# Optimization experiments

Measured on AMD Instinct MI355X. Metric: run time of the kernel, lower is better.

## Reference

```python
import jax, jax.numpy as jnp
import numpy as np

MARGIN = 0.075
CONF_THRESHOLD = 0.2


def setup_inputs() -> dict:
    key = jax.random.key(0)
    k1, k2, k3 = jax.random.split(key, 3)
    N, D = 32768, 256
    embeddings = jax.random.normal(k1, (N, D), dtype=jnp.float32)
    tags = jax.random.randint(k2, (N,), 0, 500, dtype=jnp.int64)
    confidences = jax.random.uniform(k3, (N,), dtype=jnp.float32)
    return {"embeddings": embeddings, "tags": tags, "confidences": confidences}


def _safe_sqrt(sq):
    # gradient-safe sqrt: zero at sq<=0 (matches d(0)=0, avoids NaN in vjp)
    pos = sq > 0
    return jnp.where(pos, jnp.sqrt(jnp.where(pos, sq, 1.0)), 0.0)


def _triplet_hard_mining(emb, labels):
    n = emb.shape[0]
    # pairwise euclidean distances (cdist p=2)
    sq_norm = jnp.sum(emb * emb, axis=1)  # [n]
    sq = sq_norm[:, None] + sq_norm[None, :] - 2.0 * (emb @ emb.T)
    dist = _safe_sqrt(jnp.maximum(sq, 0.0))  # [n, n]

    same = labels[:, None] == labels[None, :]
    eye = jnp.eye(n, dtype=bool)
    pos_mask = same & ~eye
    neg_mask = ~same

    inf = jnp.float32(jnp.inf)
    hard_pos = jnp.max(jnp.where(pos_mask, dist, -inf), axis=1)  # [n]
    neg_min = jnp.min(jnp.where(neg_mask, dist, inf), axis=1)    # [n]
    # semi-hard negatives: neg dists strictly greater than hardest positive
    shn_mask = neg_mask & (dist > hard_pos[:, None])
    shn_min = jnp.min(jnp.where(shn_mask, dist, inf), axis=1)
    hard_neg = jnp.where(jnp.isfinite(shn_min), shn_min, neg_min)

    valid = jnp.any(pos_mask, axis=1) & jnp.any(neg_mask, axis=1)
    per_anchor = jax.nn.relu(hard_pos - hard_neg + MARGIN)
    per_anchor = jnp.where(valid, per_anchor, 0.0)
    cnt = jnp.sum(valid.astype(jnp.float32))
    # if no valid anchors (also covers <2 unique labels), loss is 0
    return jnp.where(cnt > 0, jnp.sum(per_anchor) / jnp.maximum(cnt, 1.0), 0.0)


def reference(embeddings, tags, confidences):
    n = embeddings.shape[0]
    top_k = int(CONF_THRESHOLD * n)
    _, idx = jax.lax.top_k(confidences, top_k)
    emb = embeddings[idx]
    labels = tags[idx]
    return _triplet_hard_mining(emb, labels)
```

## Files before the change

### kernel.cpp

```cpp
#include <hip/hip_runtime.h>
#include <math.h>

#define D 256
#define MARGIN 0.075f
#define MAXM 96

typedef __bf16 bf8_t __attribute__((ext_vector_type(8)));
typedef float f4_t __attribute__((ext_vector_type(4)));
typedef int i4_t __attribute__((ext_vector_type(4)));
typedef unsigned long long ull;

#define AS1 __attribute__((address_space(1)))
#define AS3 __attribute__((address_space(3)))
static __device__ __forceinline__ void gload_lds16(const void* g, void* s) {
    __builtin_amdgcn_global_load_lds((const AS1 unsigned int*)g, (AS3 unsigned int*)s, 16, 0, 0);
}

static __device__ __forceinline__ unsigned short f2bf(float x) {
    unsigned u = __float_as_uint(x);
    unsigned r = (u + 0x7fffu + ((u >> 16) & 1u)) >> 16;
    return (unsigned short)r;
}

static __device__ __forceinline__ float dec_min(unsigned cm) {
    return (cm == 0u) ? __builtin_inff() : __uint_as_float(~cm);
}

static __device__ __forceinline__ float rmin16(float v) {
    int s;
    s = __builtin_amdgcn_update_dpp(__float_as_int(v), __float_as_int(v), 0x101, 0xF, 0xF, false);
    v = fminf(v, __int_as_float(s));
    s = __builtin_amdgcn_update_dpp(__float_as_int(v), __float_as_int(v), 0x102, 0xF, 0xF, false);
    v = fminf(v, __int_as_float(s));
    s = __builtin_amdgcn_update_dpp(__float_as_int(v), __float_as_int(v), 0x104, 0xF, 0xF, false);
    v = fminf(v, __int_as_float(s));
    s = __builtin_amdgcn_update_dpp(__float_as_int(v), __float_as_int(v), 0x108, 0xF, 0xF, false);
    v = fminf(v, __int_as_float(s));
    return v;
}

__global__ __launch_bounds__(256) void k_histscan(const float* __restrict__ conf,
                                                  int n, int ksel,
                                                  unsigned* __restrict__ h1,
                                                  unsigned* __restrict__ ctrl) {
    int t = threadIdx.x;
    int i = blockIdx.x * 256 + t;
    if (i < n) atomicAdd(&h1[__float_as_uint(conf[i]) >> 16], 1u);
    __threadfence();
    __syncthreads();
    __shared__ unsigned sdone;
    if (t == 0) sdone = atomicAdd(&ctrl[8], 1u);
    __syncthreads();
    if (sdone != gridDim.x - 1) return;
    __threadfence();
    __shared__ unsigned part[256], sfx[256];
    __shared__ int schunk;
    unsigned k = (unsigned)ksel;
    unsigned s = 0;
    const uint4* h4 = (const uint4*)(h1 + t * 256);
    #pragma unroll
    for (int b = 0; b < 64; b++) { uint4 v = h4[b]; s += v.x + v.y + v.z + v.w; }
    part[t] = s;
    __syncthreads();
    for (int off = 1; off < 256; off <<= 1) {
        unsigned v = (t + off < 256) ? part[t + off] : 0u;
        __syncthreads();
        part[t] += v;
        __syncthreads();
    }
    if (part[t] >= k && (t == 255 || part[t + 1] < k)) schunk = t;
    __syncthreads();
    int c = schunk;
    unsigned above = (c == 255) ? 0u : part[c + 1];
    sfx[t] = h1[c * 256 + t];
    __syncthreads();
    for (int off = 1; off < 256; off <<= 1) {
        unsigned v = (t + off < 256) ? sfx[t + off] : 0u;
        __syncthreads();
        sfx[t] += v;
        __syncthreads();
    }
    if (above + sfx[t] >= k && (t == 255 || above + sfx[t + 1] < k)) {
        unsigned gt = above + ((t == 255) ? 0u : sfx[t + 1]);
        ctrl[3] = (unsigned)(c * 256 + t);
        ctrl[1] = gt;
        ctrl[2] = k - gt;
    }
}

__global__ __launch_bounds__(256) void k_selrank(const float* __restrict__ conf, int n,
                                                 unsigned* __restrict__ ctrl,
                                                 int* __restrict__ idx_sel,
                                                 ull* __restrict__ cand) {
    int t = threadIdx.x;
    int i = blockIdx.x * 256 + t;
    unsigned b16 = ctrl[3];
    if (i < n) {
        unsigned u = __float_as_uint(conf[i]);
        unsigned t16 = u >> 16;
        if (t16 > b16) {
            unsigned pos = atomicAdd(&ctrl[5], 1u);
            idx_sel[pos] = i;
        } else if (t16 == b16) {
            unsigned pos = atomicAdd(&ctrl[6], 1u);
            __hip_atomic_store(&cand[pos], ((ull)u << 32) | (unsigned)i,
                               __ATOMIC_RELAXED, __HIP_MEMORY_SCOPE_AGENT);
        }
    }
    __threadfence();
    __syncthreads();
    __shared__ unsigned sdone;
    if (t == 0) sdone = atomicAdd(&ctrl[9], 1u);
    __syncthreads();
    if (sdone != gridDim.x - 1) return;
    __threadfence();

    __shared__ ull scand[1024];
    int M = (int)__hip_atomic_load(&ctrl[6], __ATOMIC_RELAXED, __HIP_MEMORY_SCOPE_AGENT);
    unsigned need = ctrl[2], cgt = ctrl[1];
    bool useLds = (M <= 1024);
    if (useLds) {
        for (int m = t; m < M; m += 256)
            scand[m] = __hip_atomic_load(&cand[m], __ATOMIC_RELAXED, __HIP_MEMORY_SCOPE_AGENT);
        __syncthreads();
    }
    for (int j = t; j < M; j += 256) {
        ull cj = useLds ? scand[j]
                        : __hip_atomic_load(&cand[j], __ATOMIC_RELAXED, __HIP_MEMORY_SCOPE_AGENT);
        unsigned uj = (unsigned)(cj >> 32);
        unsigned rank = 0;
        for (int m = 0; m < M; m++) {
            ull cm = useLds ? scand[m]
                            : __hip_atomic_load(&cand[m], __ATOMIC_RELAXED, __HIP_MEMORY_SCOPE_AGENT);
            unsigned um = (unsigned)(cm >> 32);
            if (um > uj || (um == uj && cm < cj)) rank++;
        }
        if (rank < need) idx_sel[cgt + rank] = (int)(unsigned)(cj & 0xFFFFFFFFu);
    }
}

__global__ void k_gather(const float* __restrict__ emb, const int* __restrict__ tags,
                         const int* __restrict__ idx_sel, int ksel, int np,
                         unsigned short* __restrict__ ebf, float* __restrict__ sqn,
                         int* __restrict__ lsel, unsigned* __restrict__ labhist,
                         int* __restrict__ members) {
    int j = blockIdx.x;
    int t = threadIdx.x;
    if (j < ksel) {
        int src = idx_sel[j];
        float4 v = *(const float4*)&emb[(size_t)src * D + t * 4];
        ushort4 o;
        o.x = f2bf(v.x); o.y = f2bf(v.y); o.z = f2bf(v.z); o.w = f2bf(v.w);
        *(ushort4*)&ebf[(size_t)j * D + t * 4] = o;
        float s = v.x * v.x + v.y * v.y + v.z * v.z + v.w * v.w;
        for (int off = 32; off > 0; off >>= 1) s += __shfl_down(s, off);
        if (t == 0) {
            int lab = tags[src];
            sqn[j] = s; lsel[j] = lab;
            unsigned slot = atomicAdd(&labhist[lab], 1u);
            if (slot < MAXM) members[lab * MAXM + slot] = j;
        }
    } else {
        ushort4 z = {0, 0, 0, 0};
        *(ushort4*)&ebf[(size_t)j * D + t * 4] = z;
        if (t == 0) { sqn[j] = __builtin_inff(); lsel[j] = -1; }
    }
}

__global__ __launch_bounds__(256) void k_hardpos(const unsigned short* __restrict__ ebf,
                                                 const float* __restrict__ sqn,
                                                 const int* __restrict__ members,
                                                 const unsigned* __restrict__ labhist,
                                                 unsigned* __restrict__ hp_g) {
    int L = blockIdx.x;
    int t = threadIdx.x;
    int m = (int)labhist[L];
    if (m > MAXM) m = MAXM;
    if (m < 2) return;

    __shared__ unsigned short rows[MAXM * 256];
    __shared__ float lsqn[MAXM];
    __shared__ unsigned hpl[MAXM];
    __shared__ int ridx[MAXM];

    for (int a = t; a < m; a += 256) {
        int r = members[L * MAXM + a];
        ridx[a] = r; lsqn[a] = sqn[r]; hpl[a] = 0u;
    }
    __syncthreads();
    for (int e = t * 8; e < m * 256; e += 256 * 8) {
        int a = e >> 8, c = e & 255;
        *(uint4*)&rows[a * 256 + c] = *(const uint4*)&ebf[(size_t)ridx[a] * D + c];
    }
    __syncthreads();

    int npair = m * (m - 1) / 2;
    for (int pidx = t; pidx < npair; pidx += 256) {
        int a = 0, rem = pidx;
        while (rem >= m - 1 - a) { rem -= m - 1 - a; a++; }
        int b = a + 1 + rem;
        const unsigned* ra = (const unsigned*)&rows[a * 256];
        const unsigned* rb = (const unsigned*)&rows[b * 256];
        float dot = 0.f;
        #pragma unroll 8
        for (int c = 0; c < 128; c++) {
            unsigned ua = ra[c], ub = rb[c];
            float a0 = __uint_as_float(ua << 16);
            float a1 = __uint_as_float(ua & 0xFFFF0000u);
            float b0 = __uint_as_float(ub << 16);
            float b1 = __uint_as_float(ub & 0xFFFF0000u);
            dot = fmaf(a0, b0, dot);
            dot = fmaf(a1, b1, dot);
        }
        float dsq = fmaxf(lsqn[a] + lsqn[b] - 2.f * dot, 0.f);
        unsigned bits = __float_as_uint(dsq);
        atomicMax(&hpl[a], bits);
        atomicMax(&hpl[b], bits);
    }
    __syncthreads();
    for (int a = t; a < m; a += 256) hp_g[ridx[a]] = hpl[a];
}

__global__ __launch_bounds__(256, 3) void k_fused(const unsigned short* __restrict__ Ebf,
                                                  const float* __restrict__ sqn,
                                                  const int* __restrict__ lsel,
                                                  const unsigned* __restrict__ hp_g,
                                                  unsigned* __restrict__ nm_g,
                                                  unsigned* __restrict__ shn_g,
                                                  int np, int nb, int ksel) {
    int rem = blockIdx.x, bi = 0;
    while (rem >= nb - bi) { rem -= nb - bi; bi++; }
    int bj = bi + rem;
    int i0 = bi * 128, j0 = bj * 128;
    bool diag = (bi == bj);

    __shared__ __align__(16) char smem[32768];
    char* ldsA = smem;
    char* ldsB = smem + 16384;

    int t = threadIdx.x;
    int w = t >> 6, l = t & 63;
    int wm = w & 1, wn = w >> 1;
    int lr = l & 15, lq = l >> 4;
    int r7 = lr & 7, rh = lr >> 3;

    int dr = l >> 3;
    int sg = (l & 7) ^ dr;
    const unsigned short* gA = Ebf + (size_t)(i0 + dr) * D + sg * 8;
    const unsigned short* gB = Ebf + (size_t)(j0 + dr) * D + sg * 8;

    f4_t zero = {0.f, 0.f, 0.f, 0.f};
    f4_t acc[4][4];
    #pragma unroll
    for (int p = 0; p < 4; p++)
        #pragma unroll
        for (int q = 0; q < 4; q++) acc[p][q] = zero;

    for (int k0 = 0; k0 < D; k0 += 64) {
        #pragma unroll
        for (int c = 0; c < 4; c++) {
            int R0 = w * 32 + c * 8;
            gload_lds16(gA + (size_t)R0 * D + k0, ldsA + R0 * 128);
            gload_lds16(gB + (size_t)R0 * D + k0, ldsB + R0 * 128);
        }
        __syncthreads();
        #pragma unroll
        for (int ks8 = 0; ks8 < 8; ks8 += 4) {
            bf8_t a[4], b[4];
            #pragma unroll
            for (int p = 0; p < 4; p++) {
                int off = ((wm * 8 + p * 2 + rh) << 10) + ((r7 * 8 + ((ks8 + lq) ^ r7)) << 4);
                a[p] = *(const bf8_t*)(ldsA + off);
            }
            #pragma unroll
            for (int q = 0; q < 4; q++) {
                int off = ((wn * 8 + q * 2 + rh) << 10) + ((r7 * 8 + ((ks8 + lq) ^ r7)) << 4);
                b[q] = *(const bf8_t*)(ldsB + off);
            }
            #pragma unroll
            for (int p = 0; p < 4; p++)
                #pragma unroll
                for (int q = 0; q < 4; q++)
                    acc[p][q] = __builtin_amdgcn_mfma_f32_16x16x32_bf16(a[p], b[q], acc[p][q], 0, 0, 0);
        }
        __syncthreads();
    }

    float* sqnA = (float*)smem;
    float* sqnB = sqnA + 128;
    int* labA = (int*)(sqnB + 128);
    int* labB = labA + 128;
    float* thrA = (float*)(labB + 128);
    float* thrB = thrA + 128;
    if (t < 128) {
        float s = sqn[i0 + t];
        sqnA[t] = s; labA[t] = lsel[i0 + t];
        thrA[t] = __uint_as_float(hp_g[i0 + t]) - s;
    } else {
        int u = t - 128;
        float s = sqn[j0 + u];
        sqnB[u] = s; labB[u] = lsel[j0 + u];
        thrB[u] = __uint_as_float(hp_g[j0 + u]) - s;
    }
    __syncthreads();

    const float INF = __builtin_inff();
    int colL[4], ljv[4];
    float sBq[4], thrBq[4];
    #pragma unroll
    for (int q = 0; q < 4; q++) {
        colL[q] = wn * 64 + q * 16 + lr;
        ljv[q] = labB[colL[q]];
        sBq[q] = sqnB[colL[q]];
        thrBq[q] = thrB[colL[q]];
    }
    f4_t sqA4[4], thrA4[4];
    i4_t labA4[4];
    #pragma unroll
    for (int p = 0; p < 4; p++) {
        int rb = wm * 64 + p * 16 + lq * 4;
        sqA4[p] = *(const f4_t*)&sqnA[rb];
        thrA4[p] = *(const f4_t*)&thrA[rb];
        labA4[p] = *(const i4_t*)&labA[rb];
    }

    #pragma unroll
    for (int p = 0; p < 4; p++) {
        #pragma unroll
        for (int r = 0; r < 4; r++) {
            int li = labA4[p][r];
            float thr = thrA4[p][r];
            float nmv = INF, smv = INF;
            #pragma unroll
            for (int q = 0; q < 4; q++) {
                float v = fmaf(-2.f, acc[p][q][r], sBq[q]);
                v = (ljv[q] == li) ? INF : v;
                nmv = fminf(nmv, v);
                smv = fminf(smv, (v > thr) ? v : INF);
            }
            nmv = rmin16(nmv);
            smv = rmin16(smv);
            if (lr == 0) {
                int gm = i0 + wm * 64 + p * 16 + lq * 4 + r;
                float sqi = sqA4[p][r];
                if (nmv < INF)
                    atomicMax(&nm_g[gm], ~__float_as_uint(fmaxf(sqi + nmv, 0.f)));
                if (smv < INF)
                    atomicMax(&shn_g[gm], ~__float_as_uint(fmaxf(sqi + smv, 0.f)));
            }
        }
    }

    if (!diag) {
        #pragma unroll
        for (int q = 0; q < 4; q++) {
            int lj = ljv[q];
            float thrc = thrBq[q];
            float nmv = INF, smv = INF;
            #pragma unroll
            for (int p = 0; p < 4; p++)
                #pragma unroll
                for (int r = 0; r < 4; r++) {
                    float w2 = fmaf(-2.f, acc[p][q][r], sqA4[p][r]);
                    w2 = (labA4[p][r] == lj) ? INF : w2;
                    nmv = fminf(nmv, w2);
                    smv = fminf(smv, (w2 > thrc) ? w2 : INF);
                }
            nmv = fminf(nmv, __shfl_xor(nmv, 16));
            nmv = fminf(nmv, __shfl_xor(nmv, 32));
            smv = fminf(smv, __shfl_xor(smv, 16));
            smv = fminf(smv, __shfl_xor(smv, 32));
            if (lq == 0) {
                int gn = j0 + colL[q];
                if (nmv < INF)
                    atomicMax(&nm_g[gn], ~__float_as_uint(fmaxf(sBq[q] + nmv, 0.f)));
                if (smv < INF)
                    atomicMax(&shn_g[gn], ~__float_as_uint(fmaxf(sBq[q] + smv, 0.f)));
            }
        }
    }
}

__global__ __launch_bounds__(256) void k_loss(const unsigned* __restrict__ hp,
                                              const unsigned* __restrict__ nm,
                                              const unsigned* __restrict__ shn,
                                              const int* __restrict__ lsel,
                                              const unsigned* __restrict__ labhist,
                                              int ksel, float* __restrict__ fsums,
                                              unsigned* __restrict__ ctrl,
                                              float* __restrict__ out) {
    __shared__ float ssum[256], scnt[256];
    int t = threadIdx.x;
    int i = blockIdx.x * 256 + t;
    float sum = 0.f, cnt = 0.f;
    if (i < ksel) {
        int li = lsel[i];
        unsigned h = labhist[li];
        bool valid = (h >= 2u) && ((unsigned)ksel > h);
        float hp2 = __uint_as_float(hp[i]);
        float nm2 = dec_min(nm[i]);
        float sh2 = dec_min(shn[i]);
        float hn2 = isinf(sh2) ? nm2 : sh2;
        float lv = valid ? fmaxf(sqrtf(hp2) - sqrtf(hn2) + MARGIN, 0.f) : 0.f;
        sum = lv;
        cnt = valid ? 1.f : 0.f;
    }
    ssum[t] = sum; scnt[t] = cnt;
    __syncthreads();
    for (int off = 128; off > 0; off >>= 1) {
        if (t < off) { ssum[t] += ssum[t + off]; scnt[t] += scnt[t + off]; }
        __syncthreads();
    }
    if (t == 0) {
        atomicAdd(&fsums[0], ssum[0]);
        atomicAdd(&fsums[1], scnt[0]);
        __threadfence();
        unsigned done = atomicAdd(&ctrl[7], 1u);
        if (done == gridDim.x - 1) {
            float s = atomicAdd(&fsums[0], 0.f);
            float c = atomicAdd(&fsums[1], 0.f);
            out[0] = (c > 0.f) ? (s / fmaxf(c, 1.f)) : 0.f;
        }
    }
}

__global__ void k_wsfail(float* out, float code) { out[0] = code; }

static inline size_t align_up(size_t x, size_t a) { return (x + a - 1) & ~(a - 1); }

extern "C" void kernel_launch(void* const* d_in, const int* in_sizes, int n_in,
                              void* d_out, int out_size, void* d_ws, size_t ws_size,
                              hipStream_t stream) {
    const float* emb  = (const float*)d_in[0];
    const int*   tags = (const int*)d_in[1];
    const float* conf = (const float*)d_in[2];
    float* out = (float*)d_out;

    int n = in_sizes[2];
    int ksel = (int)(0.2 * (double)n);
    int np = ((ksel + 127) / 128) * 128;
    int nb = np / 128;
    int nlab = 512;

    size_t off = 0;
    size_t o_ctrl = off; off = align_up(off + 32 * sizeof(unsigned), 256);
    size_t o_fs   = off; off = align_up(off + 8 * sizeof(float), 256);
    size_t o_lh   = off; off = align_up(off + (size_t)nlab * 4, 256);
    size_t o_hp   = off; off = align_up(off + (size_t)np * 4, 256);
    size_t o_nm   = off; off = align_up(off + (size_t)np * 4, 256);
    size_t o_shn  = off; off = align_up(off + (size_t)np * 4, 256);
    size_t o_h1   = off; off = align_up(off + 65536 * 4, 256);
    size_t zero_bytes = off;
    size_t o_idx  = off; off = align_up(off + (size_t)ksel * 4, 256);
    size_t o_cand = off; off = align_up(off + (size_t)n * 8, 256);
    size_t o_mem  = off; off = align_up(off + (size_t)nlab * MAXM * 4, 256);
    size_t o_lab  = off; off = align_up(off + (size_t)np * 4, 256);
    size_t o_sqn  = off; off = align_up(off + (size_t)np * 4, 256);
    size_t o_ebf  = off; off = align_up(off + (size_t)np * D * 2, 256);

    if (ws_size < off) {
        k_wsfail<<<1, 1, 0, stream>>>(out, -(float)(ws_size >> 20));
        return;
    }

    char* ws = (char*)d_ws;
    unsigned*       ctrl    = (unsigned*)(ws + o_ctrl);
    float*          fsums   = (float*)(ws + o_fs);
    unsigned*       labhist = (unsigned*)(ws + o_lh);
    unsigned*       hp_g    = (unsigned*)(ws + o_hp);
    unsigned*       nm_g    = (unsigned*)(ws + o_nm);
    unsigned*       shn_g   = (unsigned*)(ws + o_shn);
    unsigned*       h1      = (unsigned*)(ws + o_h1);
    int*            idx_sel = (int*)(ws + o_idx);
    ull*            cand    = (ull*)(ws + o_cand);
    int*            members = (int*)(ws + o_mem);
    int*            lsel    = (int*)(ws + o_lab);
    float*          sqn     = (float*)(ws + o_sqn);
    unsigned short* ebf     = (unsigned short*)(ws + o_ebf);

    hipMemsetAsync(d_ws, 0, zero_bytes, stream);
    int selgrid = (n + 255) / 256;
    k_histscan<<<selgrid, 256, 0, stream>>>(conf, n, ksel, h1, ctrl);
    k_selrank<<<selgrid, 256, 0, stream>>>(conf, n, ctrl, idx_sel, cand);
    k_gather<<<np, 64, 0, stream>>>(emb, tags, idx_sel, ksel, np, ebf, sqn, lsel,
                                    labhist, members);
    k_hardpos<<<512, 256, 0, stream>>>(ebf, sqn, members, labhist, hp_g);
    int ntri = nb * (nb + 1) / 2;
    k_fused<<<ntri, 256, 0, stream>>>(ebf, sqn, lsel, hp_g, nm_g, shn_g, np, nb, ksel);
    k_loss<<<(ksel + 255) / 256, 256, 0, stream>>>(hp_g, nm_g, shn_g, lsel, labhist,
                                                   ksel, fsums, ctrl, out);
}
```

Measured before the change: 194.4 us.

## Widen selection blocks, serialize fine-bin scan, move per-row zeroing into gather

```diff
diff --git a/kernel.cpp b/kernel.cpp
--- a/kernel.cpp
+++ b/kernel.cpp
@@ -39,12 +39,12 @@
     return v;
 }
 
-__global__ __launch_bounds__(256) void k_histscan(const float* __restrict__ conf,
-                                                  int n, int ksel,
-                                                  unsigned* __restrict__ h1,
-                                                  unsigned* __restrict__ ctrl) {
+__global__ __launch_bounds__(1024) void k_histscan(const float* __restrict__ conf,
+                                                   int n, int ksel,
+                                                   unsigned* __restrict__ h1,
+                                                   unsigned* __restrict__ ctrl) {
     int t = threadIdx.x;
-    int i = blockIdx.x * 256 + t;
+    int i = blockIdx.x * 1024 + t;
     if (i < n) atomicAdd(&h1[__float_as_uint(conf[i]) >> 16], 1u);
     __threadfence();
     __syncthreads();
@@ -53,47 +53,44 @@
     __syncthreads();
     if (sdone != gridDim.x - 1) return;
     __threadfence();
-    __shared__ unsigned part[256], sfx[256];
+    __shared__ unsigned part[1024];
     __shared__ int schunk;
     unsigned k = (unsigned)ksel;
     unsigned s = 0;
-    const uint4* h4 = (const uint4*)(h1 + t * 256);
+    const uint4* h4 = (const uint4*)(h1 + t * 64);
     #pragma unroll
-    for (int b = 0; b < 64; b++) { uint4 v = h4[b]; s += v.x + v.y + v.z + v.w; }
+    for (int b = 0; b < 16; b++) { uint4 v = h4[b]; s += v.x + v.y + v.z + v.w; }
     part[t] = s;
     __syncthreads();
-    for (int off = 1; off < 256; off <<= 1) {
-        unsigned v = (t + off < 256) ? part[t + off] : 0u;
+    for (int off = 1; off < 1024; off <<= 1) {
+        unsigned v = (t + off < 1024) ? part[t + off] : 0u;
         __syncthreads();
         part[t] += v;
         __syncthreads();
     }
-    if (part[t] >= k && (t == 255 || part[t + 1] < k)) schunk = t;
-    __syncthreads();
-    int c = schunk;
-    unsigned above = (c == 255) ? 0u : part[c + 1];
-    sfx[t] = h1[c * 256 + t];
-    __syncthreads();
-    for (int off = 1; off < 256; off <<= 1) {
-        unsigned v = (t + off < 256) ? sfx[t + off] : 0u;
-        __syncthreads();
-        sfx[t] += v;
-        __syncthreads();
-    }
-    if (above + sfx[t] >= k && (t == 255 || above + sfx[t + 1] < k)) {
-        unsigned gt = above + ((t == 255) ? 0u : sfx[t + 1]);
-        ctrl[3] = (unsigned)(c * 256 + t);
-        ctrl[1] = gt;
-        ctrl[2] = k - gt;
-    }
-}
-
-__global__ __launch_bounds__(256) void k_selrank(const float* __restrict__ conf, int n,
-                                                 unsigned* __restrict__ ctrl,
-                                                 int* __restrict__ idx_sel,
-                                                 ull* __restrict__ cand) {
+    if (part[t] >= k && (t == 1023 || part[t + 1] < k)) schunk = t;
+    __syncthreads();
+    if (t == 0) {
+        int c = schunk;
+        unsigned cum = (c == 1023) ? 0u : part[c + 1];
+        int bin = 0; unsigned rem = 1;
+        for (int b = 63; b >= 0; b--) {
+            unsigned h = h1[c * 64 + b];
+            if (cum + h >= k) { bin = c * 64 + b; rem = k - cum; break; }
+            cum += h;
+        }
+        ctrl[3] = (unsigned)bin;
+        ctrl[1] = k - rem;
+        ctrl[2] = rem;
+    }
+}
+
+__global__ __launch_bounds__(1024) void k_selrank(const float* __restrict__ conf, int n,
+                                                  unsigned* __restrict__ ctrl,
+                                                  int* __restrict__ idx_sel,
+                                                  ull* __restrict__ cand) {
     int t = threadIdx.x;
-    int i = blockIdx.x * 256 + t;
+    int i = blockIdx.x * 1024 + t;
     unsigned b16 = ctrl[3];
     if (i < n) {
         unsigned u = __float_as_uint(conf[i]);
@@ -120,11 +117,11 @@
     unsigned need = ctrl[2], cgt = ctrl[1];
     bool useLds = (M <= 1024);
     if (useLds) {
-        for (int m = t; m < M; m += 256)
+        for (int m = t; m < M; m += 1024)
             scand[m] = __hip_atomic_load(&cand[m], __ATOMIC_RELAXED, __HIP_MEMORY_SCOPE_AGENT);
         __syncthreads();
     }
-    for (int j = t; j < M; j += 256) {
+    for (int j = t; j < M; j += 1024) {
         ull cj = useLds ? scand[j]
                         : __hip_atomic_load(&cand[j], __ATOMIC_RELAXED, __HIP_MEMORY_SCOPE_AGENT);
         unsigned uj = (unsigned)(cj >> 32);
@@ -139,31 +136,43 @@
     }
 }
 
-__global__ void k_gather(const float* __restrict__ emb, const int* __restrict__ tags,
-                         const int* __restrict__ idx_sel, int ksel, int np,
-                         unsigned short* __restrict__ ebf, float* __restrict__ sqn,
-                         int* __restrict__ lsel, unsigned* __restrict__ labhist,
-                         int* __restrict__ members) {
-    int j = blockIdx.x;
+__global__ __launch_bounds__(256) void k_gather(const float* __restrict__ emb,
+                                                const int* __restrict__ tags,
+                                                const int* __restrict__ idx_sel,
+                                                int ksel, int np,
+                                                unsigned short* __restrict__ ebf,
+                                                float* __restrict__ sqn,
+                                                int* __restrict__ lsel,
+                                                unsigned* __restrict__ labhist,
+                                                int* __restrict__ members,
+                                                unsigned* __restrict__ hp_g,
+                                                unsigned* __restrict__ nm_g,
+                                                unsigned* __restrict__ shn_g) {
     int t = threadIdx.x;
+    int j = blockIdx.x * 4 + (t >> 6);
+    int lane = t & 63;
     if (j < ksel) {
         int src = idx_sel[j];
-        float4 v = *(const float4*)&emb[(size_t)src * D + t * 4];
+        float4 v = *(const float4*)&emb[(size_t)src * D + lane * 4];
         ushort4 o;
         o.x = f2bf(v.x); o.y = f2bf(v.y); o.z = f2bf(v.z); o.w = f2bf(v.w);
-        *(ushort4*)&ebf[(size_t)j * D + t * 4] = o;
+        *(ushort4*)&ebf[(size_t)j * D + lane * 4] = o;
         float s = v.x * v.x + v.y * v.y + v.z * v.z + v.w * v.w;
         for (int off = 32; off > 0; off >>= 1) s += __shfl_down(s, off);
-        if (t == 0) {
+        if (lane == 0) {
             int lab = tags[src];
             sqn[j] = s; lsel[j] = lab;
+            hp_g[j] = 0u; nm_g[j] = 0u; shn_g[j] = 0u;
             unsigned slot = atomicAdd(&labhist[lab], 1u);
             if (slot < MAXM) members[lab * MAXM + slot] = j;
         }
-    } else {
+    } else if (j < np) {
         ushort4 z = {0, 0, 0, 0};
-        *(ushort4*)&ebf[(size_t)j * D + t * 4] = z;
-        if (t == 0) { sqn[j] = __builtin_inff(); lsel[j] = -1; }
+        *(ushort4*)&ebf[(size_t)j * D + lane * 4] = z;
+        if (lane == 0) {
+            sqn[j] = __builtin_inff(); lsel[j] = -1;
+            hp_g[j] = 0u; nm_g[j] = 0u; shn_g[j] = 0u;
+        }
     }
 }
 
@@ -446,11 +455,11 @@
     size_t o_ctrl = off; off = align_up(off + 32 * sizeof(unsigned), 256);
     size_t o_fs   = off; off = align_up(off + 8 * sizeof(float), 256);
     size_t o_lh   = off; off = align_up(off + (size_t)nlab * 4, 256);
+    size_t o_h1   = off; off = align_up(off + 65536 * 4, 256);
+    size_t zero_bytes = off;
     size_t o_hp   = off; off = align_up(off + (size_t)np * 4, 256);
     size_t o_nm   = off; off = align_up(off + (size_t)np * 4, 256);
     size_t o_shn  = off; off = align_up(off + (size_t)np * 4, 256);
-    size_t o_h1   = off; off = align_up(off + 65536 * 4, 256);
-    size_t zero_bytes = off;
     size_t o_idx  = off; off = align_up(off + (size_t)ksel * 4, 256);
     size_t o_cand = off; off = align_up(off + (size_t)n * 8, 256);
     size_t o_mem  = off; off = align_up(off + (size_t)nlab * MAXM * 4, 256);
@@ -467,10 +476,10 @@
     unsigned*       ctrl    = (unsigned*)(ws + o_ctrl);
     float*          fsums   = (float*)(ws + o_fs);
     unsigned*       labhist = (unsigned*)(ws + o_lh);
+    unsigned*       h1      = (unsigned*)(ws + o_h1);
     unsigned*       hp_g    = (unsigned*)(ws + o_hp);
     unsigned*       nm_g    = (unsigned*)(ws + o_nm);
     unsigned*       shn_g   = (unsigned*)(ws + o_shn);
-    unsigned*       h1      = (unsigned*)(ws + o_h1);
     int*            idx_sel = (int*)(ws + o_idx);
     ull*            cand    = (ull*)(ws + o_cand);
     int*            members = (int*)(ws + o_mem);
@@ -479,11 +488,11 @@
     unsigned short* ebf     = (unsigned short*)(ws + o_ebf);
 
     hipMemsetAsync(d_ws, 0, zero_bytes, stream);
-    int selgrid = (n + 255) / 256;
-    k_histscan<<<selgrid, 256, 0, stream>>>(conf, n, ksel, h1, ctrl);
-    k_selrank<<<selgrid, 256, 0, stream>>>(conf, n, ctrl, idx_sel, cand);
-    k_gather<<<np, 64, 0, stream>>>(emb, tags, idx_sel, ksel, np, ebf, sqn, lsel,
-                                    labhist, members);
+    int selgrid = (n + 1023) / 1024;
+    k_histscan<<<selgrid, 1024, 0, stream>>>(conf, n, ksel, h1, ctrl);
+    k_selrank<<<selgrid, 1024, 0, stream>>>(conf, n, ctrl, idx_sel, cand);
+    k_gather<<<np / 4, 256, 0, stream>>>(emb, tags, idx_sel, ksel, np, ebf, sqn, lsel,
+                                         labhist, members, hp_g, nm_g, shn_g);
     k_hardpos<<<512, 256, 0, stream>>>(ebf, sqn, members, labhist, hp_g);
     int ntri = nb * (nb + 1) / 2;
     k_fused<<<ntri, 256, 0, stream>>>(ebf, sqn, lsel, hp_g, nm_g, shn_g, np, nb, ksel);
```

Result: slower. 200.8 us (+3.3%).
